# Optimization experiments

Measured on AMD Instinct MI355X. Metric: run time of the kernel, lower is better.

## Reference

```python
import jax, jax.numpy as jnp
import numpy as np

HEADS = 16
DIM_HEAD = 64
SCALE = DIM_HEAD ** -0.5


def setup_inputs() -> dict:
    key = jax.random.key(0)
    k1, k2, k3, k4 = jax.random.split(key, 4)
    b, n, dim = 2, 2048, 1024
    inner = HEADS * DIM_HEAD  # 1024
    x = jax.random.normal(k1, (b, n, dim), dtype=jnp.float32)
    # binary keep-mask (multiplicative, as in the original module)
    seq_mask = (jax.random.uniform(k2, (b, n)) < 0.9).astype(jnp.float32)
    # weights stored [in, out] (transpose of torch Linear layout)
    w_qkv = jax.random.normal(k3, (dim, inner * 3), dtype=jnp.float32) * (dim ** -0.5)
    w_out = jax.random.normal(k4, (inner, dim), dtype=jnp.float32) * (inner ** -0.5)
    return {"x": x, "seq_mask": seq_mask, "w_qkv": w_qkv, "w_out": w_out}


def reference(x, seq_mask, w_qkv, w_out):
    b, n, dim = x.shape
    qkv = x @ w_qkv                                   # [b, n, 3*inner]
    q, k, v = jnp.split(qkv, 3, axis=-1)
    split_heads = lambda t: t.reshape(b, n, HEADS, DIM_HEAD).transpose(0, 2, 1, 3)
    q, k, v = split_heads(q), split_heads(k), split_heads(v)  # [b, h, n, d]
    dots = jnp.einsum('bhid,bhjd->bhij', q, k) * SCALE        # [b, h, n, n]
    # multiplicative mask, broadcast over heads and query index i; mask depends on key index j
    dots = dots * seq_mask[:, None, None, :]
    attn = jax.nn.softmax(dots, axis=-1)
    out = jnp.einsum('bhij,bhjd->bhid', attn, v)              # [b, h, n, d]
    out = out.transpose(0, 2, 1, 3).reshape(b, n, HEADS * DIM_HEAD)
    return out @ w_out                                        # dropout p=0 -> identity
```

## Files before the change

### kernel.cpp

```cpp
#include <hip/hip_runtime.h>
#include <hip/hip_bf16.h>

using bf16 = __hip_bfloat16;
typedef __attribute__((ext_vector_type(8))) short short8;
typedef __attribute__((ext_vector_type(4))) float floatx4;
typedef __attribute__((ext_vector_type(16))) float floatx16;

#define MFMA_BF16(a, b, c) __builtin_amdgcn_mfma_f32_16x16x32_bf16((a), (b), (c), 0, 0, 0)
#define MFMA32(a, b, c) __builtin_amdgcn_mfma_f32_32x32x16_bf16((a), (b), (c), 0, 0, 0)

__device__ __forceinline__ void gload_lds16(const bf16* g, bf16* l) {
  __builtin_amdgcn_global_load_lds((__attribute__((address_space(1))) void*)g,
                                   (__attribute__((address_space(3))) void*)l,
                                   16, 0, 0);
}

__device__ __forceinline__ unsigned short bfbits(float f) {
  bf16 b = __float2bfloat16(f);
  return *reinterpret_cast<unsigned short*>(&b);
}

__device__ __forceinline__ int swz32(int r) { return (r & 7) ^ ((r >> 3) & 3); }

#define KSCALE 0.18033688011112042f

__global__ __launch_bounds__(256)
void probemask_k(const void* __restrict__ msrc, bf16* __restrict__ dst,
                 int* __restrict__ flag) {
  __shared__ int any;
  const int tid = threadIdx.x;
  if (tid == 0) any = 0;
  __syncthreads();
  const unsigned* mw = (const unsigned*)msrc;
  int bad = 0;
#pragma unroll
  for (int i = 0; i < 4; i++) {
    unsigned w = mw[tid * 4 + i];
    if (w != 0u && w != 0x3F800000u) bad = 1;
  }
  if (bad) atomicOr(&any, 1);
  __syncthreads();
  const int isbf = any;
  if (tid == 0) flag[0] = isbf;
  if (isbf) {
#pragma unroll
    for (int i = 0; i < 2; i++)
      ((int4*)dst)[tid * 2 + i] = ((const int4*)msrc)[tid * 2 + i];
  } else {
#pragma unroll
    for (int i = 0; i < 4; i++) {
      float4 v = ((const float4*)msrc)[tid * 4 + i];
      int o = tid * 16 + i * 4;
      dst[o + 0] = __float2bfloat16(v.x);
      dst[o + 1] = __float2bfloat16(v.y);
      dst[o + 2] = __float2bfloat16(v.z);
      dst[o + 3] = __float2bfloat16(v.w);
    }
  }
}

__global__ __launch_bounds__(256)
void cvt_k(const void* __restrict__ src, bf16* __restrict__ dst, int n,
           const int* __restrict__ flag) {
  if (*flag) return;
  int i = (blockIdx.x * 256 + threadIdx.x) * 4;
  if (i >= n) return;
  float4 v = ((const float4*)src)[i >> 2];
  dst[i + 0] = __float2bfloat16(v.x);
  dst[i + 1] = __float2bfloat16(v.y);
  dst[i + 2] = __float2bfloat16(v.z);
  dst[i + 3] = __float2bfloat16(v.w);
}

__global__ __launch_bounds__(256)
void transpose2_k(const void* __restrict__ in0, bf16* __restrict__ out0,
                  const void* __restrict__ in1, bf16* __restrict__ out1,
                  const int* __restrict__ flag) {
  __shared__ bf16 tile[32][33];
  const int isbf = *flag;
  constexpr int R = 1024;
  const void* in;
  bf16* out;
  int C, bx;
  if (blockIdx.x < 96) { in = in0; out = out0; C = 3072; bx = blockIdx.x * 32; }
  else                 { in = in1; out = out1; C = 1024; bx = (blockIdx.x - 96) * 32; }
  int by = blockIdx.y * 32;
  int tx = threadIdx.x & 31, ty = threadIdx.x >> 5;
#pragma unroll
  for (int i = 0; i < 4; i++) {
    size_t idx = (size_t)(by + ty + i * 8) * C + bx + tx;
    tile[ty + i * 8][tx] =
        isbf ? ((const bf16*)in)[idx] : __float2bfloat16(((const float*)in)[idx]);
  }
  __syncthreads();
#pragma unroll
  for (int i = 0; i < 4; i++)
    out[(size_t)(bx + ty + i * 8) * R + by + tx] = tile[tx][ty + i * 8];
}

template <int MODE>
__global__ __launch_bounds__(256, 2)
void gemm_k(const bf16* __restrict__ A, const bf16* __restrict__ Aalt,
            const bf16* __restrict__ Bt,
            bf16* __restrict__ Qo, bf16* __restrict__ Ko, bf16* __restrict__ Vo,
            void* __restrict__ Co, const bf16* __restrict__ Mk,
            const int* __restrict__ flag) {
  constexpr int K = 1024;
  __shared__ __align__(16) bf16 As[128 * 32];
  __shared__ __align__(16) bf16 Bs[128 * 32];

  const int tid = threadIdx.x;
  const int lane = tid & 63;
  const int wv = tid >> 6;
  const int wm = wv & 1, wn = wv >> 1;
  const int l15 = lane & 15, quad = lane >> 4;

  const int bm = blockIdx.y * 128;
  const int bn = blockIdx.x * 128;

  const int sml = tid >> 2;
  const int sg = (tid & 3) ^ ((sml >> 1) & 3);

  const int isbf = *flag;
  const bf16* Ab = (MODE == 0 && isbf) ? Aalt : A;

  floatx4 acc[4][4] = {};

  for (int k0 = 0; k0 < K; k0 += 32) {
    __syncthreads();
    const bf16* a0 = Ab + (size_t)(bm + sml) * K + k0 + sg * 8;
    gload_lds16(a0, &As[tid * 8]);
    gload_lds16(a0 + (size_t)64 * K, &As[2048 + tid * 8]);
    const bf16* b0 = Bt + (size_t)(bn + sml) * K + k0 + sg * 8;
    gload_lds16(b0, &Bs[tid * 8]);
    gload_lds16(b0 + (size_t)64 * K, &Bs[2048 + tid * 8]);
    __syncthreads();

    short8 af[4], bfr[4];
#pragma unroll
    for (int mi = 0; mi < 4; mi++) {
      int m = wm * 64 + mi * 16 + l15;
      af[mi] = *(const short8*)&As[m * 32 + ((quad ^ ((m >> 1) & 3)) * 8)];
    }
#pragma unroll
    for (int ni = 0; ni < 4; ni++) {
      int n = wn * 64 + ni * 16 + l15;
      bfr[ni] = *(const short8*)&Bs[n * 32 + ((quad ^ ((n >> 1) & 3)) * 8)];
    }
#pragma unroll
    for (int mi = 0; mi < 4; mi++)
#pragma unroll
      for (int ni = 0; ni < 4; ni++)
        acc[mi][ni] = MFMA_BF16(af[mi], bfr[ni], acc[mi][ni]);
  }

#pragma unroll
  for (int mi = 0; mi < 4; mi++) {
    const int row0 = bm + wm * 64 + mi * 16 + quad * 4;
#pragma unroll
    for (int ni = 0; ni < 4; ni++) {
      const int col = bn + wn * 64 + ni * 16 + l15;
      if (MODE == 0) {
        const int sec = col >> 10;
        const int cc = col & 1023;
        const int h = cc >> 6, d = cc & 63;
        const int b_idx = row0 >> 11;
        const int nn0 = row0 & 2047;
        if (sec == 0) {
          bf16* dst = Qo + (size_t)(b_idx * 16 + h) * 131072 + (size_t)nn0 * 64 + d;
#pragma unroll
          for (int r = 0; r < 4; r++) dst[r * 64] = __float2bfloat16(acc[mi][ni][r]);
        } else if (sec == 1) {
          const bf16* mrow = Mk + (size_t)b_idx * 2048 + nn0;
          bf16* dst = Ko + (size_t)(b_idx * 16 + h) * 131072 + (size_t)nn0 * 64 + d;
#pragma unroll
          for (int r = 0; r < 4; r++)
            dst[r * 64] = __float2bfloat16(acc[mi][ni][r] * KSCALE *
                                           __bfloat162float(mrow[r]));
        } else {
          bf16* dst = Vo + (size_t)(b_idx * 16 + h) * 131072 + (size_t)d * 2048 + nn0;
#pragma unroll
          for (int r = 0; r < 4; r++) dst[r] = __float2bfloat16(acc[mi][ni][r]);
        }
      } else {
        if (isbf) {
          bf16* C2 = (bf16*)Co;
#pragma unroll
          for (int r = 0; r < 4; r++)
            C2[(size_t)(row0 + r) * 1024 + col] = __float2bfloat16(acc[mi][ni][r]);
        } else {
          float* C2 = (float*)Co;
#pragma unroll
          for (int r = 0; r < 4; r++)
            C2[(size_t)(row0 + r) * 1024 + col] = acc[mi][ni][r];
        }
      }
    }
  }
}

__global__ __launch_bounds__(512, 4)
void flash_k(const bf16* __restrict__ Q, const bf16* __restrict__ K,
             const bf16* __restrict__ VT, bf16* __restrict__ AO) {
  __shared__ __align__(16) bf16 Ks[2][8192];
  __shared__ __align__(16) bf16 Vs[2][8192];

  const int tid = threadIdx.x;
  const int lane = tid & 63;
  const int l31 = lane & 31;
  const int l5h = lane >> 5;
  const int sw = swz32(l31);

  const int qt = blockIdx.x & 15;
  const int hl = blockIdx.x >> 4;
  const int b_idx = hl >> 4, h = hl & 15;
  const int w = tid >> 6;
  const int rg = w & 3;

  const bf16* Qh = Q + (size_t)hl * 131072;
  const bf16* Kh = K + (size_t)hl * 131072;
  const bf16* Vh = VT + (size_t)hl * 131072;

  const int qbase = qt * 128 + rg * 32;
  const int qrow = qbase + l31;

  short8 qf[4];
#pragma unroll
  for (int c = 0; c < 4; c++)
    qf[c] = *(const short8*)&Qh[(size_t)qrow * 64 + c * 16 + l5h * 8];

  floatx16 o_acc[2] = {};
  float rsum = 0.f;

  const int st = tid & 255;
  const int half = tid >> 8;
  const int sjj = st >> 3;
  const int sgp = (st & 7) ^ swz32(sjj);
  const int hoff = half * 4096;
  const int jh = half * 1024;
  const int choff = hoff;

  gload_lds16(&Kh[(size_t)(jh + sjj) * 64 + sgp * 8], &Ks[0][hoff + st * 8]);
  gload_lds16(&Kh[(size_t)(jh + 32 + sjj) * 64 + sgp * 8], &Ks[0][hoff + 2048 + st * 8]);
  gload_lds16(&Vh[(size_t)sjj * 2048 + jh + sgp * 8], &Vs[0][hoff + st * 8]);
  gload_lds16(&Vh[(size_t)(32 + sjj) * 2048 + jh + sgp * 8], &Vs[0][hoff + 2048 + st * 8]);

  for (int it = 0; it < 16; ++it) {
    const int b = it & 1;
    __syncthreads();
    if (it < 15) {
      const int j1 = jh + (it + 1) * 64;
      gload_lds16(&Kh[(size_t)(j1 + sjj) * 64 + sgp * 8], &Ks[b ^ 1][hoff + st * 8]);
      gload_lds16(&Kh[(size_t)(j1 + 32 + sjj) * 64 + sgp * 8], &Ks[b ^ 1][hoff + 2048 + st * 8]);
      gload_lds16(&Vh[(size_t)sjj * 2048 + j1 + sgp * 8], &Vs[b ^ 1][hoff + st * 8]);
      gload_lds16(&Vh[(size_t)(32 + sjj) * 2048 + j1 + sgp * 8], &Vs[b ^ 1][hoff + 2048 + st * 8]);
    }

    floatx16 s[2] = {};
    __builtin_amdgcn_s_setprio(1);
#pragma unroll
    for (int kt = 0; kt < 2; kt++) {
      const int key = kt * 32 + l31;
#pragma unroll
      for (int c = 0; c < 4; c++) {
        const int g = c * 2 + l5h;
        short8 kf = *(const short8*)&Ks[b][choff + key * 64 + ((g ^ sw) * 8)];
        s[kt] = MFMA32(kf, qf[c], s[kt]);
      }
    }
    __builtin_amdgcn_s_setprio(0);

    float rs0 = 0.f, rs1 = 0.f, rs2 = 0.f, rs3 = 0.f;
#pragma unroll
    for (int kt = 0; kt < 2; kt++)
#pragma unroll
      for (int r = 0; r < 16; r += 4) {
        const float p0 = __builtin_amdgcn_exp2f(s[kt][r + 0]);
        const float p1 = __builtin_amdgcn_exp2f(s[kt][r + 1]);
        const float p2 = __builtin_amdgcn_exp2f(s[kt][r + 2]);
        const float p3 = __builtin_amdgcn_exp2f(s[kt][r + 3]);
        s[kt][r + 0] = p0; rs0 += p0;
        s[kt][r + 1] = p1; rs1 += p1;
        s[kt][r + 2] = p2; rs2 += p2;
        s[kt][r + 3] = p3; rs3 += p3;
      }
    float rs = (rs0 + rs1) + (rs2 + rs3);
    rs += __shfl_xor(rs, 32, 64);
    rsum += rs;

    short8 pf[4];
#pragma unroll
    for (int c = 0; c < 4; c++) {
      const int kt = c >> 1;
      const int rb = (c & 1) * 8;
      unsigned x0, x1, y0, y1;
      asm("v_cvt_pk_bf16_f32 %0, %1, %2" : "=v"(x0) : "v"(s[kt][rb + 0]), "v"(s[kt][rb + 1]));
      asm("v_cvt_pk_bf16_f32 %0, %1, %2" : "=v"(x1) : "v"(s[kt][rb + 2]), "v"(s[kt][rb + 3]));
      asm("v_cvt_pk_bf16_f32 %0, %1, %2" : "=v"(y0) : "v"(s[kt][rb + 4]), "v"(s[kt][rb + 5]));
      asm("v_cvt_pk_bf16_f32 %0, %1, %2" : "=v"(y1) : "v"(s[kt][rb + 6]), "v"(s[kt][rb + 7]));
      asm("v_permlane32_swap_b32 %0, %1" : "+v"(x0), "+v"(y0));
      asm("v_permlane32_swap_b32 %0, %1" : "+v"(x1), "+v"(y1));
      union { unsigned u[4]; short8 v; } cv;
      cv.u[0] = x0; cv.u[1] = x1; cv.u[2] = y0; cv.u[3] = y1;
      pf[c] = cv.v;
    }

    __builtin_amdgcn_s_setprio(1);
#pragma unroll
    for (int dt = 0; dt < 2; dt++) {
      const int d = dt * 32 + l31;
#pragma unroll
      for (int c = 0; c < 4; c++) {
        const int g = c * 2 + l5h;
        short8 vf = *(const short8*)&Vs[b][choff + d * 64 + ((g ^ sw) * 8)];
        o_acc[dt] = MFMA32(vf, pf[c], o_acc[dt]);
      }
    }
    __builtin_amdgcn_s_setprio(0);
  }

  __syncthreads();
  float* cb = (float*)&Ks[0][0];
  float* rbuf = (float*)&Vs[0][0];
  if (w >= 4) {
    const int slot = (w - 4) * 64 + lane;
    float4* dst = (float4*)(cb + (size_t)slot * 32);
#pragma unroll
    for (int dt = 0; dt < 2; dt++)
#pragma unroll
      for (int q = 0; q < 4; q++) {
        float4 v = make_float4(o_acc[dt][q * 4 + 0], o_acc[dt][q * 4 + 1],
                               o_acc[dt][q * 4 + 2], o_acc[dt][q * 4 + 3]);
        dst[(dt * 4 + q) ^ (lane & 7)] = v;
      }
    rbuf[slot] = rsum;
  }
  __syncthreads();
  if (w < 4) {
    const int slot = w * 64 + lane;
    const float4* src = (const float4*)(cb + (size_t)slot * 32);
#pragma unroll
    for (int dt = 0; dt < 2; dt++)
#pragma unroll
      for (int q = 0; q < 4; q++) {
        float4 v = src[(dt * 4 + q) ^ (lane & 7)];
        o_acc[dt][q * 4 + 0] += v.x;
        o_acc[dt][q * 4 + 1] += v.y;
        o_acc[dt][q * 4 + 2] += v.z;
        o_acc[dt][q * 4 + 3] += v.w;
      }
    rsum += rbuf[slot];

    const float rinv = 1.f / rsum;
    bf16* orow = AO + (size_t)(b_idx * 2048 + qbase + l31) * 1024 + h * 64;
#pragma unroll
    for (int dt = 0; dt < 2; dt++)
#pragma unroll
      for (int rg2 = 0; rg2 < 4; rg2++) {
        ushort4 u;
        u.x = bfbits(o_acc[dt][rg2 * 4 + 0] * rinv);
        u.y = bfbits(o_acc[dt][rg2 * 4 + 1] * rinv);
        u.z = bfbits(o_acc[dt][rg2 * 4 + 2] * rinv);
        u.w = bfbits(o_acc[dt][rg2 * 4 + 3] * rinv);
        *(ushort4*)&orow[dt * 32 + rg2 * 8 + l5h * 4] = u;
      }
  }
}

extern "C" void kernel_launch(void* const* d_in, const int* in_sizes, int n_in,
                              void* d_out, int out_size, void* d_ws, size_t ws_size,
                              hipStream_t stream) {
  const void* x     = d_in[0];
  const void* mask  = d_in[1];
  const void* w_qkv = d_in[2];
  const void* w_out = d_in[3];

  bf16* ws    = (bf16*)d_ws;
  bf16* xb    = ws;
  bf16* AO    = ws;
  bf16* wqkvT = ws + 4194304;
  bf16* woutT = wqkvT + 3145728;
  bf16* Qb    = woutT + 1048576;
  bf16* Kb    = Qb + 4194304;
  bf16* maskb = Kb + 4194304;
  int*  flag  = (int*)(maskb + 4096);
  bf16* VT    = (bf16*)d_out;

  probemask_k<<<1, 256, 0, stream>>>(mask, maskb, flag);
  cvt_k<<<4096, 256, 0, stream>>>(x, xb, 4194304, flag);
  transpose2_k<<<dim3(128, 32), 256, 0, stream>>>(w_qkv, wqkvT, w_out, woutT, flag);
  gemm_k<0><<<dim3(24, 32), 256, 0, stream>>>(xb, (const bf16*)x, wqkvT, Qb, Kb, VT,
                                              nullptr, maskb, flag);
  flash_k<<<512, 512, 0, stream>>>(Qb, Kb, VT, AO);
  gemm_k<1><<<dim3(8, 32), 256, 0, stream>>>(AO, nullptr, woutT, nullptr, nullptr,
                                             nullptr, d_out, nullptr, flag);
}
```

Before: 189.8 us.

## Prepack K/V in MFMA fragment order and load them directly to registers

The QKV GEMM epilogue now writes K and V in a tiled layout that matches the MFMA 32x32 operand fragments, with a vectorized 4-wide store for V. The flash kernel drops LDS staging, double buffering and barriers. Each wave loads K/V fragments straight from global memory into registers, software-pipelining the next K tile during softmax, and processes 32 keys per iteration instead of 64. Block indices are also remapped to spread heads across XCDs. This trades LDS traffic and syncs for more redundant global/L2 reads, since the four row-group waves now each load the same K/V.

```diff
diff --git a/kernel.cpp b/kernel.cpp
--- a/kernel.cpp
+++ b/kernel.cpp
@@ -19,8 +19,6 @@
   bf16 b = __float2bfloat16(f);
   return *reinterpret_cast<unsigned short*>(&b);
 }
-
-__device__ __forceinline__ int swz32(int r) { return (r & 7) ^ ((r >> 3) & 3); }
 
 #define KSCALE 0.18033688011112042f
 
@@ -172,15 +170,26 @@
           for (int r = 0; r < 4; r++) dst[r * 64] = __float2bfloat16(acc[mi][ni][r]);
         } else if (sec == 1) {
           const bf16* mrow = Mk + (size_t)b_idx * 2048 + nn0;
-          bf16* dst = Ko + (size_t)(b_idx * 16 + h) * 131072 + (size_t)nn0 * 64 + d;
+          const int t = nn0 >> 6, kt = (nn0 >> 5) & 1, l31r = nn0 & 31;
+          const int g = d >> 3, j = d & 7;
+          bf16* dst = Ko + (size_t)(b_idx * 16 + h) * 131072 + t * 4096 + kt * 2048 +
+                      (g >> 1) * 512 + (g & 1) * 256 + l31r * 8 + j;
 #pragma unroll
           for (int r = 0; r < 4; r++)
-            dst[r * 64] = __float2bfloat16(acc[mi][ni][r] * KSCALE *
-                                           __bfloat162float(mrow[r]));
+            dst[r * 8] = __float2bfloat16(acc[mi][ni][r] * KSCALE *
+                                          __bfloat162float(mrow[r]));
         } else {
-          bf16* dst = Vo + (size_t)(b_idx * 16 + h) * 131072 + (size_t)d * 2048 + nn0;
-#pragma unroll
-          for (int r = 0; r < 4; r++) dst[r] = __float2bfloat16(acc[mi][ni][r]);
+          const int t = nn0 >> 6;
+          const int kl = nn0 & 63;
+          const int g = kl >> 3, j0 = kl & 7;
+          bf16* dst = Vo + (size_t)(b_idx * 16 + h) * 131072 + t * 4096 +
+                      (d >> 5) * 2048 + (g >> 1) * 512 + (g & 1) * 256 + (d & 31) * 8 + j0;
+          ushort4 u;
+          u.x = bfbits(acc[mi][ni][0]);
+          u.y = bfbits(acc[mi][ni][1]);
+          u.z = bfbits(acc[mi][ni][2]);
+          u.w = bfbits(acc[mi][ni][3]);
+          *(ushort4*)dst = u;
         }
       } else {
         if (isbf) {
@@ -200,26 +209,29 @@
 }
 
 __global__ __launch_bounds__(512, 4)
-void flash_k(const bf16* __restrict__ Q, const bf16* __restrict__ K,
-             const bf16* __restrict__ VT, bf16* __restrict__ AO) {
-  __shared__ __align__(16) bf16 Ks[2][8192];
-  __shared__ __align__(16) bf16 Vs[2][8192];
+void flash_k(const bf16* __restrict__ Q, const bf16* __restrict__ Kp,
+             const bf16* __restrict__ Vp, bf16* __restrict__ AO) {
+  __shared__ __align__(16) float cb[4 * 64 * 32];
+  __shared__ float rbuf[4 * 64];
 
   const int tid = threadIdx.x;
   const int lane = tid & 63;
   const int l31 = lane & 31;
   const int l5h = lane >> 5;
-  const int sw = swz32(l31);
-
-  const int qt = blockIdx.x & 15;
-  const int hl = blockIdx.x >> 4;
-  const int b_idx = hl >> 4, h = hl & 15;
   const int w = tid >> 6;
   const int rg = w & 3;
+  const int half = w >> 2;
+
+  const int bid = blockIdx.x;
+  const int wk = (bid & 7) * 64 + (bid >> 3);
+  const int qt = wk & 15;
+  const int hl = wk >> 4;
+  const int b_idx = hl >> 4, h = hl & 15;
 
   const bf16* Qh = Q + (size_t)hl * 131072;
-  const bf16* Kh = K + (size_t)hl * 131072;
-  const bf16* Vh = VT + (size_t)hl * 131072;
+  const int lo = l5h * 256 + l31 * 8;
+  const bf16* kptr = Kp + (size_t)hl * 131072 + (size_t)(half * 16) * 4096 + lo;
+  const bf16* vptr = Vp + (size_t)hl * 131072 + (size_t)(half * 16) * 4096 + lo;
 
   const int qbase = qt * 128 + rg * 32;
   const int qrow = qbase + l31;
@@ -232,96 +244,74 @@
   floatx16 o_acc[2] = {};
   float rsum = 0.f;
 
-  const int st = tid & 255;
-  const int half = tid >> 8;
-  const int sjj = st >> 3;
-  const int sgp = (st & 7) ^ swz32(sjj);
-  const int hoff = half * 4096;
-  const int jh = half * 1024;
-  const int choff = hoff;
-
-  gload_lds16(&Kh[(size_t)(jh + sjj) * 64 + sgp * 8], &Ks[0][hoff + st * 8]);
-  gload_lds16(&Kh[(size_t)(jh + 32 + sjj) * 64 + sgp * 8], &Ks[0][hoff + 2048 + st * 8]);
-  gload_lds16(&Vh[(size_t)sjj * 2048 + jh + sgp * 8], &Vs[0][hoff + st * 8]);
-  gload_lds16(&Vh[(size_t)(32 + sjj) * 2048 + jh + sgp * 8], &Vs[0][hoff + 2048 + st * 8]);
-
-  for (int it = 0; it < 16; ++it) {
-    const int b = it & 1;
-    __syncthreads();
-    if (it < 15) {
-      const int j1 = jh + (it + 1) * 64;
-      gload_lds16(&Kh[(size_t)(j1 + sjj) * 64 + sgp * 8], &Ks[b ^ 1][hoff + st * 8]);
-      gload_lds16(&Kh[(size_t)(j1 + 32 + sjj) * 64 + sgp * 8], &Ks[b ^ 1][hoff + 2048 + st * 8]);
-      gload_lds16(&Vh[(size_t)sjj * 2048 + j1 + sgp * 8], &Vs[b ^ 1][hoff + st * 8]);
-      gload_lds16(&Vh[(size_t)(32 + sjj) * 2048 + j1 + sgp * 8], &Vs[b ^ 1][hoff + 2048 + st * 8]);
-    }
-
-    floatx16 s[2] = {};
+  short8 kf[4];
+#pragma unroll
+  for (int c = 0; c < 4; c++) kf[c] = *(const short8*)(kptr + c * 512);
+
+#pragma unroll 1
+  for (int it = 0; it < 32; ++it) {
+    const int kv = it & 1;
+
+    floatx16 s = {};
     __builtin_amdgcn_s_setprio(1);
 #pragma unroll
-    for (int kt = 0; kt < 2; kt++) {
-      const int key = kt * 32 + l31;
-#pragma unroll
-      for (int c = 0; c < 4; c++) {
-        const int g = c * 2 + l5h;
-        short8 kf = *(const short8*)&Ks[b][choff + key * 64 + ((g ^ sw) * 8)];
-        s[kt] = MFMA32(kf, qf[c], s[kt]);
-      }
-    }
+    for (int c = 0; c < 4; c++) s = MFMA32(kf[c], qf[c], s);
     __builtin_amdgcn_s_setprio(0);
 
+    short8 vf[4];
+#pragma unroll
+    for (int dt = 0; dt < 2; dt++)
+#pragma unroll
+      for (int ch = 0; ch < 2; ch++)
+        vf[dt * 2 + ch] = *(const short8*)(vptr + dt * 2048 + (kv * 2 + ch) * 512);
+
+    kptr += (it < 31) ? 2048 : 0;
+#pragma unroll
+    for (int c = 0; c < 4; c++) kf[c] = *(const short8*)(kptr + c * 512);
+
     float rs0 = 0.f, rs1 = 0.f, rs2 = 0.f, rs3 = 0.f;
 #pragma unroll
-    for (int kt = 0; kt < 2; kt++)
-#pragma unroll
-      for (int r = 0; r < 16; r += 4) {
-        const float p0 = __builtin_amdgcn_exp2f(s[kt][r + 0]);
-        const float p1 = __builtin_amdgcn_exp2f(s[kt][r + 1]);
-        const float p2 = __builtin_amdgcn_exp2f(s[kt][r + 2]);
-        const float p3 = __builtin_amdgcn_exp2f(s[kt][r + 3]);
-        s[kt][r + 0] = p0; rs0 += p0;
-        s[kt][r + 1] = p1; rs1 += p1;
-        s[kt][r + 2] = p2; rs2 += p2;
-        s[kt][r + 3] = p3; rs3 += p3;
-      }
+    for (int r = 0; r < 16; r += 4) {
+      const float p0 = __builtin_amdgcn_exp2f(s[r + 0]);
+      const float p1 = __builtin_amdgcn_exp2f(s[r + 1]);
+      const float p2 = __builtin_amdgcn_exp2f(s[r + 2]);
+      const float p3 = __builtin_amdgcn_exp2f(s[r + 3]);
+      s[r + 0] = p0; rs0 += p0;
+      s[r + 1] = p1; rs1 += p1;
+      s[r + 2] = p2; rs2 += p2;
+      s[r + 3] = p3; rs3 += p3;
+    }
     float rs = (rs0 + rs1) + (rs2 + rs3);
     rs += __shfl_xor(rs, 32, 64);
     rsum += rs;
 
-    short8 pf[4];
-#pragma unroll
-    for (int c = 0; c < 4; c++) {
-      const int kt = c >> 1;
-      const int rb = (c & 1) * 8;
+    short8 pf[2];
+#pragma unroll
+    for (int ch = 0; ch < 2; ch++) {
+      const int rb = ch * 8;
       unsigned x0, x1, y0, y1;
-      asm("v_cvt_pk_bf16_f32 %0, %1, %2" : "=v"(x0) : "v"(s[kt][rb + 0]), "v"(s[kt][rb + 1]));
-      asm("v_cvt_pk_bf16_f32 %0, %1, %2" : "=v"(x1) : "v"(s[kt][rb + 2]), "v"(s[kt][rb + 3]));
-      asm("v_cvt_pk_bf16_f32 %0, %1, %2" : "=v"(y0) : "v"(s[kt][rb + 4]), "v"(s[kt][rb + 5]));
-      asm("v_cvt_pk_bf16_f32 %0, %1, %2" : "=v"(y1) : "v"(s[kt][rb + 6]), "v"(s[kt][rb + 7]));
+      asm("v_cvt_pk_bf16_f32 %0, %1, %2" : "=v"(x0) : "v"(s[rb + 0]), "v"(s[rb + 1]));
+      asm("v_cvt_pk_bf16_f32 %0, %1, %2" : "=v"(x1) : "v"(s[rb + 2]), "v"(s[rb + 3]));
+      asm("v_cvt_pk_bf16_f32 %0, %1, %2" : "=v"(y0) : "v"(s[rb + 4]), "v"(s[rb + 5]));
+      asm("v_cvt_pk_bf16_f32 %0, %1, %2" : "=v"(y1) : "v"(s[rb + 6]), "v"(s[rb + 7]));
       asm("v_permlane32_swap_b32 %0, %1" : "+v"(x0), "+v"(y0));
       asm("v_permlane32_swap_b32 %0, %1" : "+v"(x1), "+v"(y1));
       union { unsigned u[4]; short8 v; } cv;
       cv.u[0] = x0; cv.u[1] = x1; cv.u[2] = y0; cv.u[3] = y1;
-      pf[c] = cv.v;
+      pf[ch] = cv.v;
     }
 
     __builtin_amdgcn_s_setprio(1);
 #pragma unroll
-    for (int dt = 0; dt < 2; dt++) {
-      const int d = dt * 32 + l31;
-#pragma unroll
-      for (int c = 0; c < 4; c++) {
-        const int g = c * 2 + l5h;
-        short8 vf = *(const short8*)&Vs[b][choff + d * 64 + ((g ^ sw) * 8)];
-        o_acc[dt] = MFMA32(vf, pf[c], o_acc[dt]);
-      }
-    }
+    for (int dt = 0; dt < 2; dt++)
+#pragma unroll
+      for (int ch = 0; ch < 2; ch++)
+        o_acc[dt] = MFMA32(vf[dt * 2 + ch], pf[ch], o_acc[dt]);
     __builtin_amdgcn_s_setprio(0);
-  }
-
-  __syncthreads();
-  float* cb = (float*)&Ks[0][0];
-  float* rbuf = (float*)&Vs[0][0];
+
+    vptr += kv ? 4096 : 0;
+  }
+
   if (w >= 4) {
     const int slot = (w - 4) * 64 + lane;
     float4* dst = (float4*)(cb + (size_t)slot * 32);
@@ -381,17 +371,17 @@
   bf16* wqkvT = ws + 4194304;
   bf16* woutT = wqkvT + 3145728;
   bf16* Qb    = woutT + 1048576;
-  bf16* Kb    = Qb + 4194304;
-  bf16* maskb = Kb + 4194304;
+  bf16* Kp    = Qb + 4194304;
+  bf16* maskb = Kp + 4194304;
   int*  flag  = (int*)(maskb + 4096);
-  bf16* VT    = (bf16*)d_out;
+  bf16* Vp    = (bf16*)d_out;
 
   probemask_k<<<1, 256, 0, stream>>>(mask, maskb, flag);
   cvt_k<<<4096, 256, 0, stream>>>(x, xb, 4194304, flag);
   transpose2_k<<<dim3(128, 32), 256, 0, stream>>>(w_qkv, wqkvT, w_out, woutT, flag);
-  gemm_k<0><<<dim3(24, 32), 256, 0, stream>>>(xb, (const bf16*)x, wqkvT, Qb, Kb, VT,
+  gemm_k<0><<<dim3(24, 32), 256, 0, stream>>>(xb, (const bf16*)x, wqkvT, Qb, Kp, Vp,
                                               nullptr, maskb, flag);
-  flash_k<<<512, 512, 0, stream>>>(Qb, Kb, VT, AO);
+  flash_k<<<512, 512, 0, stream>>>(Qb, Kp, Vp, AO);
   gemm_k<1><<<dim3(8, 32), 256, 0, stream>>>(AO, nullptr, woutT, nullptr, nullptr,
                                              nullptr, d_out, nullptr, flag);
 }
```

Result: no change. 191.5 us (+0.9%).
